# Performance work log

Hardware: AMD Instinct MI355X
Metric: run time of the kernel (lower is better)

Reference implementation:

```python
import jax, jax.numpy as jnp
import numpy as np

H, M, D, O, N = 16, 1024, 512, 512, 16384


def setup_inputs() -> dict:
    key = jax.random.key(0)
    ks = jax.random.split(key, 8)
    inp = {
        "k": jax.random.normal(ks[0], (N, O), dtype=jnp.float32),
        "mems": jax.random.normal(ks[1], (H, M, D), dtype=jnp.float32),
        "Wk": jax.random.normal(ks[2], (H, O, D), dtype=jnp.float32) * (1.0 / np.sqrt(D)),
        "bk": jax.random.normal(ks[3], (H, O), dtype=jnp.float32) * 0.02,
        "Wv": jax.random.normal(ks[4], (H, O, D), dtype=jnp.float32) * (1.0 / np.sqrt(D)),
        "bv": jax.random.normal(ks[5], (H, O), dtype=jnp.float32) * 0.02,
        "Wf": jax.random.normal(ks[6], (O, H * O), dtype=jnp.float32) * (1.0 / np.sqrt(H * O)),
        "bf": jax.random.normal(ks[7], (O,), dtype=jnp.float32) * 0.02,
    }
    return inp


def reference(k, mems, Wk, bk, Wv, bv, Wf, bf):
    # Batched over heads. Per head h:
    #   key_h = softmax(mem_h @ Wk_h^T + bk_h)  -> [M, O]
    #   val_h = mem_h @ Wv_h^T + bv_h           -> [M, O]
    #   att_h = softmax(k @ key_h^T)            -> [N, M]
    #   out_h = att_h @ val_h                   -> [N, O]
    key_logits = jnp.einsum("hmd,hod->hmo", mems, Wk) + bk[:, None, :]
    mem_key = jax.nn.softmax(key_logits, axis=-1)            # [H, M, O]
    mem_val = jnp.einsum("hmd,hod->hmo", mems, Wv) + bv[:, None, :]  # [H, M, O]
    att = jnp.einsum("no,hmo->hnm", k, mem_key)              # [H, N, M]
    att_w = jax.nn.softmax(att, axis=-1)
    out_h = jnp.einsum("hnm,hmo->hno", att_w, mem_val)       # [H, N, O]
    # torch.cat(outputs, dim=-1): head h occupies columns [h*O:(h+1)*O]
    x = jnp.transpose(out_h, (1, 0, 2)).reshape(N, H * O)    # [N, H*O]
    return x @ Wf.T + bf                                     # [N, O]
```

## Files before the change

kernel.cpp:

```cpp
#include <hip/hip_runtime.h>
#include <hip/hip_cooperative_groups.h>
#include <math.h>

namespace cg = cooperative_groups;

typedef unsigned short u16;
typedef __attribute__((ext_vector_type(8))) short short8;
typedef __attribute__((ext_vector_type(4))) float floatx4;

#define Hh 16
#define Mm 1024
#define Dd 512
#define Oo 512
#define Nn 16384

__device__ __forceinline__ float b2f(u16 u) { return __uint_as_float(((unsigned)u) << 16); }
__device__ __forceinline__ u16 f2b(float f) {
    unsigned v = __float_as_uint(f);
    v += 0x7fffu + ((v >> 16) & 1u);
    return (u16)(v >> 16);
}
__device__ __forceinline__ short8 cvt8(const float* p) {
    float4 a = *(const float4*)p, b = *(const float4*)(p + 4);
    u16 o[8];
    o[0] = f2b(a.x); o[1] = f2b(a.y); o[2] = f2b(a.z); o[3] = f2b(a.w);
    o[4] = f2b(b.x); o[5] = f2b(b.y); o[6] = f2b(b.z); o[7] = f2b(b.w);
    return *(short8*)o;
}

__global__ __launch_bounds__(256) void gemm_bt(
    const void* __restrict__ A, const void* __restrict__ B, const float* __restrict__ bias,
    void* __restrict__ C, int K, int lda, int ldb, int ldc,
    long sA, long sB, long sBias, long sC, int aF32, int bF32, int outBf)
{
    __shared__ u16 At[64][72];
    __shared__ u16 Bt[64][72];
    const int tid = threadIdx.x, lane = tid & 63, wid = tid >> 6;
    const int m0 = blockIdx.y * 64, n0 = blockIdx.x * 64;
    const int h = blockIdx.z;
    const int wm = wid >> 1, wn = wid & 1;
    const int rl = lane & 15, rq = (lane >> 4) * 4, gl8 = (lane >> 4) * 8;

    floatx4 zero4 = {0.f, 0.f, 0.f, 0.f};
    floatx4 acc[2][2];
    acc[0][0] = zero4; acc[0][1] = zero4; acc[1][0] = zero4; acc[1][1] = zero4;

    for (int k0 = 0; k0 < K; k0 += 64) {
#pragma unroll
        for (int i = 0; i < 2; i++) {
            int c = tid + i * 256;
            int r = c >> 3, cc = (c & 7) * 8;
            long aoff = (long)h * sA + (long)(m0 + r) * lda + k0 + cc;
            long boff = (long)h * sB + (long)(n0 + r) * ldb + k0 + cc;
            *(short8*)&At[r][cc] = aF32 ? cvt8((const float*)A + aoff)
                                        : *(const short8*)((const u16*)A + aoff);
            *(short8*)&Bt[r][cc] = bF32 ? cvt8((const float*)B + boff)
                                        : *(const short8*)((const u16*)B + boff);
        }
        __syncthreads();
#pragma unroll
        for (int ks = 0; ks < 2; ks++) {
            short8 a0 = *(const short8*)&At[wm * 32 + rl][ks * 32 + gl8];
            short8 a1 = *(const short8*)&At[wm * 32 + 16 + rl][ks * 32 + gl8];
            short8 b0 = *(const short8*)&Bt[wn * 32 + rl][ks * 32 + gl8];
            short8 b1 = *(const short8*)&Bt[wn * 32 + 16 + rl][ks * 32 + gl8];
            acc[0][0] = __builtin_amdgcn_mfma_f32_16x16x32_bf16(a0, b0, acc[0][0], 0, 0, 0);
            acc[0][1] = __builtin_amdgcn_mfma_f32_16x16x32_bf16(a0, b1, acc[0][1], 0, 0, 0);
            acc[1][0] = __builtin_amdgcn_mfma_f32_16x16x32_bf16(a1, b0, acc[1][0], 0, 0, 0);
            acc[1][1] = __builtin_amdgcn_mfma_f32_16x16x32_bf16(a1, b1, acc[1][1], 0, 0, 0);
        }
        __syncthreads();
    }

#pragma unroll
    for (int i = 0; i < 2; i++)
#pragma unroll
        for (int j = 0; j < 2; j++) {
            int col = n0 + wn * 32 + j * 16 + rl;
            float bb = bias ? bias[(long)h * sBias + col] : 0.f;
#pragma unroll
            for (int r = 0; r < 4; r++) {
                int row = m0 + wm * 32 + i * 16 + rq + r;
                long idx = (long)h * sC + (long)row * ldc + col;
                float v = acc[i][j][r] + bb;
                if (outBf) ((u16*)C)[idx] = f2b(v);
                else       ((float*)C)[idx] = v;
            }
        }
}

__global__ __launch_bounds__(256) void softmax_rows(const float* __restrict__ L, u16* __restrict__ Kout)
{
    const int tid = threadIdx.x, lane = tid & 63, wid = tid >> 6;
    const long row = (long)blockIdx.x * 4 + wid;
    const float* p = L + row * 512 + lane * 8;
    float v[8];
    *(float4*)&v[0] = *(const float4*)p;
    *(float4*)&v[4] = *(const float4*)(p + 4);
    float mx = v[0];
#pragma unroll
    for (int i = 1; i < 8; i++) mx = fmaxf(mx, v[i]);
    for (int d = 1; d < 64; d <<= 1) mx = fmaxf(mx, __shfl_xor(mx, d));
    float s = 0.f;
#pragma unroll
    for (int i = 0; i < 8; i++) { v[i] = __expf(v[i] - mx); s += v[i]; }
    for (int d = 1; d < 64; d <<= 1) s += __shfl_xor(s, d);
    float inv = 1.f / s;
    u16 o[8];
#pragma unroll
    for (int i = 0; i < 8; i++) o[i] = f2b(v[i] * inv);
    *(short8*)(Kout + row * 512 + lane * 8) = *(short8*)o;
}

#define LDQ 520
#define LDP 520
#define FLASH_LDS ((64 * LDQ + 64 * LDP) * 2 + 8 * 64 * 4 + 64 * 4)

__global__ __launch_bounds__(512, 2) void flash(
    const float* __restrict__ kq, const u16* __restrict__ key,
    const u16* __restrict__ vpt, const float* __restrict__ bfv, float* __restrict__ out)
{
    cg::grid_group grid = cg::this_grid();
    extern __shared__ u16 sm[];
    u16* kq_s = sm;
    u16* Ph   = sm + 64 * LDQ;
    float* lpart = (float*)(sm + 64 * (LDQ + LDP));
    float* lfin  = lpart + 8 * 64;

    const int tid = threadIdx.x, lane = tid & 63, wid = tid >> 6;
    const int n0 = blockIdx.x * 64;
    const int rl = lane & 15, rq = (lane >> 4) * 4, gl8 = (lane >> 4) * 8;

#pragma unroll
    for (int i = 0; i < 8; i++) {
        int c = tid + i * 512;
        int r = c >> 6, cc = (c & 63) * 8;
        *(short8*)&kq_s[r * LDQ + cc] = cvt8(&kq[(long)(n0 + r) * 512 + cc]);
    }
    __syncthreads();

    floatx4 zero4 = {0.f, 0.f, 0.f, 0.f};
    floatx4 oacc[4][4], utmp[4][4];
#pragma unroll
    for (int i = 0; i < 4; i++)
#pragma unroll
        for (int j = 0; j < 4; j++) { oacc[i][j] = zero4; utmp[i][j] = zero4; }

    for (int h = 0; h < Hh; h++) {
        const u16* keyh = key + (long)h * Mm * Oo;
        const u16* vph = vpt + (long)h * Oo * Mm;

        for (int hf = 0; hf < 2; hf++) {
            float psum[4][4];
#pragma unroll
            for (int qt = 0; qt < 4; qt++)
#pragma unroll
                for (int r = 0; r < 4; r++) psum[qt][r] = 0.f;

            for (int t = 0; t < 4; t++) {
                int mb = hf * 512 + wid * 64 + t * 16;
                const u16* bp = keyh + (long)(mb + rl) * 512 + gl8;
                floatx4 s[4];
#pragma unroll
                for (int qt = 0; qt < 4; qt++) s[qt] = zero4;
#pragma unroll
                for (int ks = 0; ks < 16; ks++) {
                    short8 b = *(const short8*)(bp + ks * 32);
#pragma unroll
                    for (int qt = 0; qt < 4; qt++) {
                        short8 a = *(const short8*)&kq_s[(qt * 16 + rl) * LDQ + ks * 32 + gl8];
                        s[qt] = __builtin_amdgcn_mfma_f32_16x16x32_bf16(a, b, s[qt], 0, 0, 0);
                    }
                }
                int colP = wid * 64 + t * 16 + rl;
#pragma unroll
                for (int qt = 0; qt < 4; qt++)
#pragma unroll
                    for (int r = 0; r < 4; r++) {
                        float e = __expf(s[qt][r]);
                        psum[qt][r] += e;
                        Ph[(qt * 16 + rq + r) * LDP + colP] = f2b(e);
                    }
            }
            for (int d = 1; d < 16; d <<= 1)
#pragma unroll
                for (int qt = 0; qt < 4; qt++)
#pragma unroll
                    for (int r = 0; r < 4; r++) psum[qt][r] += __shfl_xor(psum[qt][r], d);
            if (rl == 0) {
#pragma unroll
                for (int qt = 0; qt < 4; qt++)
#pragma unroll
                    for (int r = 0; r < 4; r++) {
                        int row = qt * 16 + rq + r;
                        if (hf == 0) lpart[wid * 64 + row] = psum[qt][r];
                        else         lpart[wid * 64 + row] += psum[qt][r];
                    }
            }
            __syncthreads();

            if (hf == 1 && tid < 64) {
                float sum = 0.f;
#pragma unroll
                for (int w = 0; w < 8; w++) sum += lpart[w * 64 + tid];
                lfin[tid] = sum;
            }

            const u16* vbp[4];
#pragma unroll
            for (int ot = 0; ot < 4; ot++)
                vbp[ot] = vph + (long)(wid * 64 + ot * 16 + rl) * Mm + hf * 512 + gl8;
#pragma unroll 4
            for (int mk = 0; mk < 16; mk++) {
                short8 a[4], b[4];
#pragma unroll
                for (int qt = 0; qt < 4; qt++)
                    a[qt] = *(const short8*)&Ph[(qt * 16 + rl) * LDP + mk * 32 + gl8];
#pragma unroll
                for (int ot = 0; ot < 4; ot++)
                    b[ot] = *(const short8*)(vbp[ot] + mk * 32);
#pragma unroll
                for (int qt = 0; qt < 4; qt++)
#pragma unroll
                    for (int ot = 0; ot < 4; ot++)
                        utmp[qt][ot] = __builtin_amdgcn_mfma_f32_16x16x32_bf16(a[qt], b[ot], utmp[qt][ot], 0, 0, 0);
            }
            __syncthreads();

            if (hf == 1) {
#pragma unroll
                for (int qt = 0; qt < 4; qt++)
#pragma unroll
                    for (int r = 0; r < 4; r++) {
                        float inv = 1.f / lfin[qt * 16 + rq + r];
#pragma unroll
                        for (int ot = 0; ot < 4; ot++) {
                            oacc[qt][ot][r] += inv * utmp[qt][ot][r];
                            utmp[qt][ot][r] = 0.f;
                        }
                    }
            }
        }

        if (h < Hh - 1) grid.sync();
    }

#pragma unroll
    for (int qt = 0; qt < 4; qt++)
#pragma unroll
        for (int ot = 0; ot < 4; ot++) {
            int col = wid * 64 + ot * 16 + rl;
            float add = bfv[col];
#pragma unroll
            for (int r = 0; r < 4; r++) {
                int row = n0 + qt * 16 + rq + r;
                out[(long)row * 512 + col] = oacc[qt][ot][r] + add;
            }
        }
}

extern "C" void kernel_launch(void* const* d_in, const int* in_sizes, int n_in,
                              void* d_out, int out_size, void* d_ws, size_t ws_size,
                              hipStream_t stream)
{
    const float* k    = (const float*)d_in[0];
    const void*  mems = d_in[1];
    const void*  Wk   = d_in[2];
    const float* bk   = (const float*)d_in[3];
    const void*  Wv   = d_in[4];
    const float* bv   = (const float*)d_in[5];
    const void*  Wf   = d_in[6];
    const float* bfv  = (const float*)d_in[7];
    float* out = (float*)d_out;

    char* ws = (char*)d_ws;
    float* logits = (float*)ws;
    u16* keyb = (u16*)(ws + (size_t)Hh * Mm * Oo * 4);
    u16* valb = keyb + (size_t)Hh * Mm * Oo;
    u16* vptb = valb + (size_t)Hh * Mm * Oo;

    gemm_bt<<<dim3(8, 16, 16), 256, 0, stream>>>(
        mems, Wk, bk, logits, 512, 512, 512, 512,
        (long)Mm * Dd, (long)Oo * Dd, 512L, (long)Mm * Oo, 1, 1, 0);

    softmax_rows<<<dim3(Hh * Mm / 4), 256, 0, stream>>>(logits, keyb);

    gemm_bt<<<dim3(8, 16, 16), 256, 0, stream>>>(
        mems, Wv, bv, valb, 512, 512, 512, 512,
        (long)Mm * Dd, (long)Oo * Dd, 512L, (long)Mm * Oo, 1, 1, 1);

    gemm_bt<<<dim3(16, 8, 16), 256, 0, stream>>>(
        Wf, valb, nullptr, vptb, 512, Hh * Oo, 512, 1024,
        512L, (long)Mm * Oo, 0L, (long)Oo * Mm, 1, 0, 1);

    void* kargs[] = { (void*)&k, (void*)&keyb, (void*)&vptb, (void*)&bfv, (void*)&out };
    hipLaunchCooperativeKernel((void*)flash, dim3(Nn / 64), dim3(512),
                               kargs, (unsigned)FLASH_LDS, stream);
}
```

Baseline: 1.791 ms.

## Drop grid sync, pair key tiles in QK loop, swizzle P tile in LDS

Removes the per-head cooperative grid.sync and launches flash as a normal kernel, since blocks work on independent rows. The QK^T loop now handles two 16-row key tiles per iteration, sharing each LDS A-fragment load across two MFMAs. P writes and reads in LDS use an XOR column swizzle to cut bank conflicts on the strided scalar stores. Each change adds register pressure or index math, and the sync removal relies on the grid barrier being unnecessary for correctness.

Result: faster. 1.527 ms (-14.7%).

```diff
diff --git a/kernel.cpp b/kernel.cpp
--- a/kernel.cpp
+++ b/kernel.cpp
@@ -1,8 +1,5 @@
 #include <hip/hip_runtime.h>
-#include <hip/hip_cooperative_groups.h>
 #include <math.h>
-
-namespace cg = cooperative_groups;
 
 typedef unsigned short u16;
 typedef __attribute__((ext_vector_type(8))) short short8;
@@ -120,7 +117,6 @@
     const float* __restrict__ kq, const u16* __restrict__ key,
     const u16* __restrict__ vpt, const float* __restrict__ bfv, float* __restrict__ out)
 {
-    cg::grid_group grid = cg::this_grid();
     extern __shared__ u16 sm[];
     u16* kq_s = sm;
     u16* Ph   = sm + 64 * LDQ;
@@ -130,6 +126,7 @@
     const int tid = threadIdx.x, lane = tid & 63, wid = tid >> 6;
     const int n0 = blockIdx.x * 64;
     const int rl = lane & 15, rq = (lane >> 4) * 4, gl8 = (lane >> 4) * 8;
+    const int swzr = ((rl >> 2) & 3) << 4;
 
 #pragma unroll
     for (int i = 0; i < 8; i++) {
@@ -157,29 +154,36 @@
 #pragma unroll
                 for (int r = 0; r < 4; r++) psum[qt][r] = 0.f;
 
-            for (int t = 0; t < 4; t++) {
-                int mb = hf * 512 + wid * 64 + t * 16;
-                const u16* bp = keyh + (long)(mb + rl) * 512 + gl8;
-                floatx4 s[4];
-#pragma unroll
-                for (int qt = 0; qt < 4; qt++) s[qt] = zero4;
+            for (int tp = 0; tp < 2; tp++) {
+                int mb0 = hf * 512 + wid * 64 + tp * 32;
+                const u16* bp0 = keyh + (long)(mb0 + rl) * 512 + gl8;
+                const u16* bp1 = bp0 + 16 * 512;
+                floatx4 s0[4], s1[4];
+#pragma unroll
+                for (int qt = 0; qt < 4; qt++) { s0[qt] = zero4; s1[qt] = zero4; }
 #pragma unroll
                 for (int ks = 0; ks < 16; ks++) {
-                    short8 b = *(const short8*)(bp + ks * 32);
+                    short8 b0 = *(const short8*)(bp0 + ks * 32);
+                    short8 b1 = *(const short8*)(bp1 + ks * 32);
 #pragma unroll
                     for (int qt = 0; qt < 4; qt++) {
                         short8 a = *(const short8*)&kq_s[(qt * 16 + rl) * LDQ + ks * 32 + gl8];
-                        s[qt] = __builtin_amdgcn_mfma_f32_16x16x32_bf16(a, b, s[qt], 0, 0, 0);
+                        s0[qt] = __builtin_amdgcn_mfma_f32_16x16x32_bf16(a, b0, s0[qt], 0, 0, 0);
+                        s1[qt] = __builtin_amdgcn_mfma_f32_16x16x32_bf16(a, b1, s1[qt], 0, 0, 0);
                     }
                 }
-                int colP = wid * 64 + t * 16 + rl;
+                int colP0 = wid * 64 + tp * 32 + rl;
 #pragma unroll
                 for (int qt = 0; qt < 4; qt++)
 #pragma unroll
                     for (int r = 0; r < 4; r++) {
-                        float e = __expf(s[qt][r]);
-                        psum[qt][r] += e;
-                        Ph[(qt * 16 + rq + r) * LDP + colP] = f2b(e);
+                        int row = qt * 16 + rq + r;
+                        int swz = ((row >> 2) & 3) << 4;
+                        float e0 = __expf(s0[qt][r]);
+                        float e1 = __expf(s1[qt][r]);
+                        psum[qt][r] += e0 + e1;
+                        Ph[row * LDP + (colP0 ^ swz)] = f2b(e0);
+                        Ph[row * LDP + ((colP0 + 16) ^ swz)] = f2b(e1);
                     }
             }
             for (int d = 1; d < 16; d <<= 1)
@@ -215,7 +219,7 @@
                 short8 a[4], b[4];
 #pragma unroll
                 for (int qt = 0; qt < 4; qt++)
-                    a[qt] = *(const short8*)&Ph[(qt * 16 + rl) * LDP + mk * 32 + gl8];
+                    a[qt] = *(const short8*)&Ph[(qt * 16 + rl) * LDP + ((mk * 32 + gl8) ^ swzr)];
 #pragma unroll
                 for (int ot = 0; ot < 4; ot++)
                     b[ot] = *(const short8*)(vbp[ot] + mk * 32);
@@ -241,8 +245,6 @@
                     }
             }
         }
-
-        if (h < Hh - 1) grid.sync();
     }
 
 #pragma unroll
@@ -293,7 +295,5 @@
         Wf, valb, nullptr, vptb, 512, Hh * Oo, 512, 1024,
         512L, (long)Mm * Oo, 0L, (long)Oo * Mm, 1, 0, 1);
 
-    void* kargs[] = { (void*)&k, (void*)&keyb, (void*)&vptb, (void*)&bfv, (void*)&out };
-    hipLaunchCooperativeKernel((void*)flash, dim3(Nn / 64), dim3(512),
-                               kargs, (unsigned)FLASH_LDS, stream);
-}
+    flash<<<dim3(Nn / 64), 512, FLASH_LDS, stream>>>(k, keyb, vptb, bfv, out);
+}
```
